# Optimization experiments

Measured on AMD Instinct MI355X. Metric: run time of the kernel, lower is better.

Reference implementation:

```python
import jax, jax.numpy as jnp
import numpy as np

N, E, G, S = 200000, 800000, 2048, 128
NUM_OPS, NUM_ETYPES, NUMERIC = 64, 4, 12
H, TEXT, VOCAB, OUT = 256, 64, 30000, 512
IN0 = 32 + NUMERIC  # 44


def _ln(h, eps=1e-5):
    # nn.LayerNorm with default (ones/zeros) affine, created fresh each forward
    m = h.mean(-1, keepdims=True)
    v = ((h - m) ** 2).mean(-1, keepdims=True)
    return (h - m) * jax.lax.rsqrt(v + eps)


def _leaky(v):
    return jnp.where(v > 0, v, 0.1 * v)  # LeakyReLU(0.1)


def setup_inputs() -> dict:
    key = jax.random.key(0)
    ks = jax.random.split(key, 40)
    x = jax.random.normal(ks[0], (N, 1 + NUMERIC), jnp.float32)
    x = x.at[:, 0].set(jax.random.randint(ks[1], (N,), 0, NUM_OPS).astype(jnp.float32))
    inp = {
        'x': x,
        'edge_index': jax.random.randint(ks[2], (2, E), 0, N),
        'edge_attr': jax.random.randint(ks[3], (E,), 0, NUM_ETYPES),
        'batch': jnp.sort(jax.random.randint(ks[4], (N,), 0, G)),
        'sql_ids': jax.random.randint(ks[5], (G, S), 0, VOCAB),
        'sql_mask': (jax.random.uniform(ks[6], (G, S)) > 0.3).astype(jnp.float32),
        'op_embed': jax.random.normal(ks[7], (NUM_OPS, 32), jnp.float32),
        'edge_embed': jax.random.normal(ks[8], (NUM_ETYPES, 16), jnp.float32),
        'token_embed': jax.random.normal(ks[9], (VOCAB, TEXT), jnp.float32).at[0].set(0.0),  # padding_idx=0
    }
    dims = [IN0, H, H]
    k = 10
    for i, d in enumerate(dims):
        inp[f'lin_w{i}'] = jax.random.normal(ks[k], (d, 16), jnp.float32) * 0.05; k += 1
        inp[f'lin_b{i}'] = jnp.zeros((d,), jnp.float32)
        inp[f'eps{i}'] = jnp.zeros((), jnp.float32)  # train_eps init 0
        inp[f'W1_{i}'] = jax.random.normal(ks[k], (H, d), jnp.float32) * 0.05; k += 1
        inp[f'b1_{i}'] = jnp.zeros((H,), jnp.float32)
        inp[f'W2_{i}'] = jax.random.normal(ks[k], (H, H), jnp.float32) * 0.05; k += 1
        inp[f'b2_{i}'] = jnp.zeros((H,), jnp.float32)
    inp['mW1'] = jax.random.normal(ks[k], (H, H + 3 + TEXT), jnp.float32) * 0.05; k += 1
    inp['mb1'] = jnp.zeros((H,), jnp.float32)
    inp['mW2'] = jax.random.normal(ks[k], (OUT, H), jnp.float32) * 0.05
    inp['mb2'] = jnp.zeros((OUT,), jnp.float32)
    return inp


def reference(x, edge_index, edge_attr, batch, sql_ids, sql_mask,
              op_embed, edge_embed, token_embed,
              lin_w0, lin_b0, eps0, W1_0, b1_0, W2_0, b2_0,
              lin_w1, lin_b1, eps1, W1_1, b1_1, W2_1, b2_1,
              lin_w2, lin_b2, eps2, W1_2, b1_2, W2_2, b2_2,
              mW1, mb1, mW2, mb2):
    op_ids = jnp.clip(x[:, 0].astype(jnp.int32), 0, NUM_OPS - 1)
    nums = x[:, 1:]
    e_idx = jnp.minimum(edge_attr, NUM_ETYPES - 1)  # clamp_max
    edge_emb = edge_embed[e_idx]                    # [E,16]
    h = jnp.concatenate([op_embed[op_ids], nums], 1)  # [N,44]
    src, dst = edge_index[0], edge_index[1]
    convs = [(lin_w0, lin_b0, eps0, W1_0, b1_0, W2_0, b2_0),
             (lin_w1, lin_b1, eps1, W1_1, b1_1, W2_1, b2_1),
             (lin_w2, lin_b2, eps2, W1_2, b1_2, W2_2, b2_2)]
    for (lw, lb, eps, W1, b1, W2, b2) in convs:
        h_in = h
        # GINEConv: msg = relu(x_j + Lin(edge_attr)); sum-aggregate at dst
        msg = jax.nn.relu(h[src] + edge_emb @ lw.T + lb)        # [E,d]
        aggr = jax.ops.segment_sum(msg, dst, num_segments=h.shape[0])
        z = (1.0 + eps) * h + aggr
        h = jax.nn.relu(z @ W1.T + b1) @ W2.T + b2              # conv MLP -> [N,H]
        h = _ln(h)
        h = _leaky(h + h_in) if h_in.shape[-1] == h.shape[-1] else _leaky(h)
    # graph pooling
    g = jax.ops.segment_sum(h, batch, num_segments=G)            # global_add_pool
    count = jax.ops.segment_sum(jnp.ones((h.shape[0],), h.dtype), batch, num_segments=G)
    denom = jnp.maximum(count, 1.0)                              # scatter_mean semantics
    fanout_mean = jax.ops.segment_sum(x[:, 5], batch, num_segments=G) / denom
    cost_mean = jax.ops.segment_sum(x[:, 4], batch, num_segments=G) / denom
    graph_sum = jnp.stack([count, fanout_mean, cost_mean], 1)    # [G,3]
    # text pooling (masked mean)
    emb = token_embed[sql_ids]                                   # [G,S,TEXT]
    summed = (emb * sql_mask[..., None]).sum(1)
    lengths = jnp.maximum(sql_mask.sum(1, keepdims=True), 1.0)
    text_feat = summed / lengths
    cat = jnp.concatenate([g, graph_sum, text_feat], 1)          # [G, H+3+TEXT]
    hid = _leaky(cat @ mW1.T + mb1)                              # Dropout(0.1) is identity in eval
    return hid @ mW2.T + mb2                                     # [G, OUT]
```

## Files before the change

kernel.cpp:

```cpp
#include <hip/hip_runtime.h>

#define NN 200000
#define EE 800000
#define GG 2048
#define NBLK ((NN + 255) / 256)

typedef __attribute__((ext_vector_type(8))) short short8;
typedef __attribute__((ext_vector_type(4))) float f32x4;

__device__ __forceinline__ float bf2f(ushort u){
  unsigned x = ((unsigned)u) << 16;
  return __uint_as_float(x);
}
__device__ __forceinline__ ushort f2bf(float f){
  unsigned x = __float_as_uint(f);
  x += 0x7fffu + ((x >> 16) & 1u);
  return (ushort)(x >> 16);
}
__device__ __forceinline__ void pkAddBf16(ushort* addr, unsigned val){
  asm volatile("global_atomic_pk_add_bf16 %0, %1, off" : : "v"(addr), "v"(val) : "memory");
}

__device__ __forceinline__ void swz256(const float* __restrict__ W, ushort* __restrict__ o, int idx){
  int ks = idx >> 13, rem = idx & 8191;
  int j16 = rem >> 9, rem2 = rem & 511;
  int ln = rem2 >> 3, t = rem2 & 7;
  int row = j16*16 + (ln & 15);
  int k = ks*32 + (ln >> 4)*8 + t;
  o[idx] = f2bf(W[(size_t)row*256 + k]);
}

__global__ __launch_bounds__(256) void prep_k(
    const float* __restrict__ W10, const float* __restrict__ W20,
    const float* __restrict__ W11, const float* __restrict__ W21,
    const float* __restrict__ W12, const float* __restrict__ W22,
    const float* __restrict__ lw0, const float* __restrict__ lb0,
    const float* __restrict__ lw1, const float* __restrict__ lb1,
    const float* __restrict__ lw2, const float* __restrict__ lb2,
    const float* __restrict__ eE, const float* __restrict__ mW1,
    const float* __restrict__ mW2,
    ushort* __restrict__ wb10, ushort* __restrict__ wb20,
    ushort* __restrict__ wb11, ushort* __restrict__ wb21,
    ushort* __restrict__ wb12, ushort* __restrict__ wb22,
    ushort* __restrict__ mW1b, ushort* __restrict__ mW2b,
    float* __restrict__ eb)
{
  int b = blockIdx.x, tid = threadIdx.x;
  if (b < 64){
    int idx = b*256 + tid;
    int ks = idx >> 13, rem = idx & 8191;
    int j16 = rem >> 9, rem2 = rem & 511;
    int ln = rem2 >> 3, t = rem2 & 7;
    int row = j16*16 + (ln & 15);
    int k = ks*32 + (ln >> 4)*8 + t;
    wb10[idx] = (k < 44) ? f2bf(W10[row*44 + k]) : (ushort)0;
    return;
  }
  b -= 64;
  if (b < 256){ swz256(W20, wb20, b*256+tid); return; } b -= 256;
  if (b < 256){ swz256(W11, wb11, b*256+tid); return; } b -= 256;
  if (b < 256){ swz256(W21, wb21, b*256+tid); return; } b -= 256;
  if (b < 256){ swz256(W12, wb12, b*256+tid); return; } b -= 256;
  if (b < 256){ swz256(W22, wb22, b*256+tid); return; } b -= 256;
  if (b < 384){
    int idx = b*256 + tid; int o = idx / 384, k = idx - o*384;
    mW1b[idx] = (k < 323) ? f2bf(mW1[(size_t)o*323 + k]) : (ushort)0;
    return;
  }
  b -= 384;
  if (b < 512){ int idx = b*256+tid; mW2b[idx] = f2bf(mW2[idx]); return; } b -= 512;
  int li = b >> 2, t = b & 3;
  const float* lw = (li == 0) ? lw0 : ((li == 1) ? lw1 : lw2);
  const float* lb = (li == 0) ? lb0 : ((li == 1) ? lb1 : lb2);
  int d = (li == 0) ? 44 : 256;
  float v = 0.f;
  if (tid < d){
    float a = 0.f;
    #pragma unroll
    for (int j = 0; j < 16; j++) a += eE[t*16 + j] * lw[tid*16 + j];
    v = a + lb[tid];
  }
  eb[(li*4 + t)*256 + tid] = v;
}

__global__ __launch_bounds__(256) void build_h0_k(
    const float* __restrict__ x, const float* __restrict__ opE, ushort* __restrict__ h0)
{
  int idx = blockIdx.x*256 + threadIdx.x;
  int i = idx >> 6, c = idx & 63;
  float v = 0.f;
  if (c < 32){
    int op = (int)x[(size_t)i*13];
    op = op < 0 ? 0 : (op > 63 ? 63 : op);
    v = opE[op*32 + c];
  } else if (c < 44){
    v = x[(size_t)i*13 + (c - 31)];
  }
  h0[idx] = f2bf(v);
}

__global__ __launch_bounds__(256) void deg_k(const int* __restrict__ dst, int* __restrict__ D){
  int e = blockIdx.x*256 + threadIdx.x;
  atomicAdd(&D[dst[e]], 1);
}
__global__ __launch_bounds__(256) void scan1_k(int* __restrict__ D, int* __restrict__ bsum){
  __shared__ int s[256];
  int b = blockIdx.x, t = threadIdx.x, idx = b*256 + t;
  int v = (idx < NN) ? D[idx] : 0;
  s[t] = v; __syncthreads();
  for (int off = 1; off < 256; off <<= 1){
    int u = (t >= off) ? s[t-off] : 0;
    __syncthreads();
    s[t] += u;
    __syncthreads();
  }
  if (idx < NN) D[idx] = s[t] - v;
  if (t == 255) bsum[b] = s[255];
}
__global__ __launch_bounds__(256) void scan2_k(int* __restrict__ bsum){
  __shared__ int s[256];
  __shared__ int carry;
  int t = threadIdx.x;
  if (t == 0) carry = 0;
  __syncthreads();
  for (int c0 = 0; c0 < NBLK; c0 += 256){
    int idx = c0 + t;
    int v = (idx < NBLK) ? bsum[idx] : 0;
    s[t] = v; __syncthreads();
    for (int off = 1; off < 256; off <<= 1){
      int u = (t >= off) ? s[t-off] : 0;
      __syncthreads();
      s[t] += u;
      __syncthreads();
    }
    int ex = s[t] - v + carry;
    if (idx < NBLK) bsum[idx] = ex;
    int tot = s[255];
    __syncthreads();
    if (t == 0) carry += tot;
    __syncthreads();
  }
}
__global__ __launch_bounds__(256) void scan3_k(int* __restrict__ D, const int* __restrict__ bsum){
  int b = blockIdx.x, idx = b*256 + threadIdx.x;
  if (idx < NN) D[idx] += bsum[b];
}
__global__ __launch_bounds__(256) void fill_k(const int* __restrict__ src, const int* __restrict__ dst,
                                              const int* __restrict__ et, int* __restrict__ D,
                                              int* __restrict__ csr){
  int e = blockIdx.x*256 + threadIdx.x;
  int d = dst[e];
  int t = et[e]; t = t < 3 ? t : 3;
  int pos = atomicAdd(&D[d], 1);
  csr[pos] = src[e] | (t << 18);
}

__global__ __launch_bounds__(256) void gather256_k(
    const ushort* __restrict__ h, const int* __restrict__ Dend, const int* __restrict__ csr,
    const float* __restrict__ eb, ushort* __restrict__ aggr)
{
  __shared__ float ebs[1024];
  int tid = threadIdx.x;
  for (int i = tid; i < 1024; i += 256) ebs[i] = eb[i];
  __syncthreads();
  int r = blockIdx.x*4 + (tid >> 6);
  int lane = tid & 63;
  int c = lane * 4;
  int start = (r == 0) ? 0 : Dend[r-1];
  int end = Dend[r];
  float a0 = 0.f, a1 = 0.f, a2 = 0.f, a3 = 0.f;
  for (int e = start; e < end; e++){
    int p = csr[e];
    int s = p & 0x3FFFF;
    int t = p >> 18;
    const ushort4 hv = *(const ushort4*)(h + (size_t)s*256 + c);
    const float4 ev = *(const float4*)&ebs[t*256 + c];
    float v;
    v = bf2f(hv.x) + ev.x; a0 += v > 0.f ? v : 0.f;
    v = bf2f(hv.y) + ev.y; a1 += v > 0.f ? v : 0.f;
    v = bf2f(hv.z) + ev.z; a2 += v > 0.f ? v : 0.f;
    v = bf2f(hv.w) + ev.w; a3 += v > 0.f ? v : 0.f;
  }
  ushort4 o; o.x = f2bf(a0); o.y = f2bf(a1); o.z = f2bf(a2); o.w = f2bf(a3);
  *(ushort4*)(aggr + (size_t)r*256 + c) = o;
}

__global__ __launch_bounds__(256) void gather44_k(
    const ushort* __restrict__ h0, const int* __restrict__ Dend, const int* __restrict__ csr,
    const float* __restrict__ eb, ushort* __restrict__ aggr)
{
  __shared__ float ebs[256];
  int tid = threadIdx.x;
  if (tid < 256) ebs[tid] = eb[(tid >> 6)*256 + (tid & 63)];
  __syncthreads();
  int wv = tid >> 6, lane = tid & 63;
  int sub = lane >> 4, lg = lane & 15;
  int r = blockIdx.x*16 + wv*4 + sub;
  int c = lg * 4;
  int start = (r == 0) ? 0 : Dend[r-1];
  int end = Dend[r];
  float a0 = 0.f, a1 = 0.f, a2 = 0.f, a3 = 0.f;
  for (int e = start; e < end; e++){
    int p = csr[e];
    int s = p & 0x3FFFF;
    int t = p >> 18;
    const ushort4 hv = *(const ushort4*)(h0 + (size_t)s*64 + c);
    const float4 ev = *(const float4*)&ebs[t*64 + c];
    float v;
    v = bf2f(hv.x) + ev.x; a0 += v > 0.f ? v : 0.f;
    v = bf2f(hv.y) + ev.y; a1 += v > 0.f ? v : 0.f;
    v = bf2f(hv.z) + ev.z; a2 += v > 0.f ? v : 0.f;
    v = bf2f(hv.w) + ev.w; a3 += v > 0.f ? v : 0.f;
  }
  ushort4 o; o.x = f2bf(a0); o.y = f2bf(a1); o.z = f2bf(a2); o.w = f2bf(a3);
  *(ushort4*)(aggr + (size_t)r*64 + c) = o;
}

__global__ __launch_bounds__(256) void msg44_k(
    const ushort* __restrict__ h0, const int* __restrict__ src, const int* __restrict__ dst,
    const int* __restrict__ et, const float* __restrict__ eb, ushort* __restrict__ aggr)
{
  int e = blockIdx.x*4 + (threadIdx.x >> 6);
  int lane = threadIdx.x & 63;
  if (lane < 22){
    int s = src[e], d = dst[e];
    int t = et[e]; t = t < 3 ? t : 3;
    int c = lane * 2;
    const ushort2 hv = *(const ushort2*)(h0 + (size_t)s*64 + c);
    float v0 = bf2f(hv.x) + eb[t*256 + c];     v0 = v0 > 0.f ? v0 : 0.f;
    float v1 = bf2f(hv.y) + eb[t*256 + c + 1]; v1 = v1 > 0.f ? v1 : 0.f;
    unsigned pv = (unsigned)f2bf(v0) | ((unsigned)f2bf(v1) << 16);
    pkAddBf16(aggr + (size_t)d*64 + c, pv);
  }
}
__global__ __launch_bounds__(256) void msg256_k(
    const ushort* __restrict__ h, const int* __restrict__ src, const int* __restrict__ dst,
    const int* __restrict__ et, const float* __restrict__ eb, ushort* __restrict__ aggr)
{
  int e = blockIdx.x*4 + (threadIdx.x >> 6);
  int lane = threadIdx.x & 63;
  int s = src[e], d = dst[e];
  int t = et[e]; t = t < 3 ? t : 3;
  int c = lane * 4;
  const ushort4 hv = *(const ushort4*)(h + (size_t)s*256 + c);
  const float4 ev = *(const float4*)(eb + t*256 + c);
  float v0 = bf2f(hv.x) + ev.x; v0 = v0 > 0.f ? v0 : 0.f;
  float v1 = bf2f(hv.y) + ev.y; v1 = v1 > 0.f ? v1 : 0.f;
  float v2 = bf2f(hv.z) + ev.z; v2 = v2 > 0.f ? v2 : 0.f;
  float v3 = bf2f(hv.w) + ev.w; v3 = v3 > 0.f ? v3 : 0.f;
  unsigned p0 = (unsigned)f2bf(v0) | ((unsigned)f2bf(v1) << 16);
  unsigned p1 = (unsigned)f2bf(v2) | ((unsigned)f2bf(v3) << 16);
  ushort* ap = aggr + (size_t)d*256 + c;
  pkAddBf16(ap, p0);
  pkAddBf16(ap + 2, p1);
}

template<int KD, int RESID>
__global__ __launch_bounds__(256) void layer_k(
    const ushort* hsrc, const ushort* __restrict__ aggr,
    const ushort* __restrict__ W1s, const float* __restrict__ b1,
    const ushort* __restrict__ W2s, const float* __restrict__ b2,
    const float* __restrict__ epsp, ushort* hout)
{
  __shared__ ushort ZT[64][264];
  __shared__ float red1[64][4], red2[64][4], mnL[64], rsL[64];
  const int tid = threadIdx.x, lane = tid & 63, wv = tid >> 6;
  const int l15 = lane & 15, lq = lane >> 4;
  const int rowBase = blockIdx.x * 64;
  const float epv = 1.0f + epsp[0];

  if (KD == 256){
    #pragma unroll
    for (int p = 0; p < 16; p++){
      int r = p*4 + (tid >> 6);
      int c = (tid & 63) * 4;
      const ushort4 hv = *(const ushort4*)(hsrc + (size_t)(rowBase + r)*256 + c);
      const ushort4 av = *(const ushort4*)(aggr + (size_t)(rowBase + r)*256 + c);
      ushort4 o;
      o.x = f2bf(epv*bf2f(hv.x) + bf2f(av.x));
      o.y = f2bf(epv*bf2f(hv.y) + bf2f(av.y));
      o.z = f2bf(epv*bf2f(hv.z) + bf2f(av.z));
      o.w = f2bf(epv*bf2f(hv.w) + bf2f(av.w));
      *(ushort4*)&ZT[r][c] = o;
    }
  } else {
    #pragma unroll
    for (int p = 0; p < 4; p++){
      int r = p*16 + (tid >> 4);
      int c = (tid & 15) * 4;
      const ushort4 hv = *(const ushort4*)(hsrc + (size_t)(rowBase + r)*64 + c);
      const ushort4 av = *(const ushort4*)(aggr + (size_t)(rowBase + r)*64 + c);
      ushort4 o;
      o.x = f2bf(epv*bf2f(hv.x) + bf2f(av.x));
      o.y = f2bf(epv*bf2f(hv.y) + bf2f(av.y));
      o.z = f2bf(epv*bf2f(hv.z) + bf2f(av.z));
      o.w = f2bf(epv*bf2f(hv.w) + bf2f(av.w));
      *(ushort4*)&ZT[r][c] = o;
    }
  }
  __syncthreads();

  f32x4 acc[4][4];
  #pragma unroll
  for (int i = 0; i < 4; i++)
    #pragma unroll
    for (int j = 0; j < 4; j++){ f32x4 z = {0.f,0.f,0.f,0.f}; acc[i][j] = z; }

  #pragma unroll
  for (int s = 0; s < KD/32; s++){
    short8 af[4], bfv[4];
    #pragma unroll
    for (int j = 0; j < 4; j++)
      bfv[j] = *(const short8*)(W1s + ((size_t)(s*16 + wv*4 + j)*64 + lane)*8);
    #pragma unroll
    for (int i = 0; i < 4; i++)
      af[i] = *(const short8*)&ZT[i*16 + l15][s*32 + lq*8];
    #pragma unroll
    for (int i = 0; i < 4; i++)
      #pragma unroll
      for (int j = 0; j < 4; j++)
        acc[i][j] = __builtin_amdgcn_mfma_f32_16x16x32_bf16(af[i], bfv[j], acc[i][j], 0, 0, 0);
  }
  __syncthreads();

  {
    float b1c[4];
    #pragma unroll
    for (int j = 0; j < 4; j++) b1c[j] = b1[wv*64 + j*16 + l15];
    #pragma unroll
    for (int i = 0; i < 4; i++)
      #pragma unroll
      for (int j = 0; j < 4; j++){
        int cc = wv*64 + j*16 + l15;
        #pragma unroll
        for (int rg = 0; rg < 4; rg++){
          int r = i*16 + (lq << 2) + rg;
          float v = acc[i][j][rg] + b1c[j];
          v = v > 0.f ? v : 0.f;
          ZT[r][cc] = f2bf(v);
        }
      }
  }
  __syncthreads();

  #pragma unroll
  for (int i = 0; i < 4; i++)
    #pragma unroll
    for (int j = 0; j < 4; j++){ f32x4 z = {0.f,0.f,0.f,0.f}; acc[i][j] = z; }

  #pragma unroll
  for (int s = 0; s < 8; s++){
    short8 af[4], bfv[4];
    #pragma unroll
    for (int j = 0; j < 4; j++)
      bfv[j] = *(const short8*)(W2s + ((size_t)(s*16 + wv*4 + j)*64 + lane)*8);
    #pragma unroll
    for (int i = 0; i < 4; i++)
      af[i] = *(const short8*)&ZT[i*16 + l15][s*32 + lq*8];
    #pragma unroll
    for (int i = 0; i < 4; i++)
      #pragma unroll
      for (int j = 0; j < 4; j++)
        acc[i][j] = __builtin_amdgcn_mfma_f32_16x16x32_bf16(af[i], bfv[j], acc[i][j], 0, 0, 0);
  }

  float b2c[4];
  #pragma unroll
  for (int j = 0; j < 4; j++) b2c[j] = b2[wv*64 + j*16 + l15];
  #pragma unroll
  for (int i = 0; i < 4; i++){
    #pragma unroll
    for (int rg = 0; rg < 4; rg++){
      float s1 = 0.f, s2 = 0.f;
      #pragma unroll
      for (int j = 0; j < 4; j++){
        float y = acc[i][j][rg] + b2c[j];
        s1 += y; s2 += y*y;
      }
      #pragma unroll
      for (int m = 1; m < 16; m <<= 1){
        s1 += __shfl_xor(s1, m, 64);
        s2 += __shfl_xor(s2, m, 64);
      }
      if (l15 == 0){
        int r = i*16 + (lq << 2) + rg;
        red1[r][wv] = s1; red2[r][wv] = s2;
      }
    }
  }
  __syncthreads();
  if (tid < 64){
    float s1 = red1[tid][0] + red1[tid][1] + red1[tid][2] + red1[tid][3];
    float s2 = red2[tid][0] + red2[tid][1] + red2[tid][2] + red2[tid][3];
    float mn = s1 * (1.f/256.f);
    float vr = s2 * (1.f/256.f) - mn*mn;
    mnL[tid] = mn;
    rsL[tid] = rsqrtf(vr + 1e-5f);
  }
  __syncthreads();
  #pragma unroll
  for (int i = 0; i < 4; i++){
    #pragma unroll
    for (int rg = 0; rg < 4; rg++){
      int r = i*16 + (lq << 2) + rg;
      float mn = mnL[r], rs = rsL[r];
      #pragma unroll
      for (int j = 0; j < 4; j++){
        int cc = wv*64 + j*16 + l15;
        float y = acc[i][j][rg] + b2c[j];
        float v = (y - mn) * rs;
        if (RESID) v += bf2f(hsrc[(size_t)(rowBase + r)*256 + cc]);
        v = v > 0.f ? v : 0.1f*v;
        ZT[r][cc] = f2bf(v);
      }
    }
  }
  __syncthreads();
  #pragma unroll
  for (int p = 0; p < 16; p++){
    int r = p*4 + (tid >> 6);
    int c = (tid & 63) * 4;
    *(ushort4*)(hout + (size_t)(rowBase + r)*256 + c) = *(const ushort4*)&ZT[r][c];
  }
}

__global__ __launch_bounds__(256) void readout_k(
    const ushort* __restrict__ h, const int* __restrict__ batch, const float* __restrict__ x,
    const int* __restrict__ sqlIds, const float* __restrict__ sqlMask,
    const float* __restrict__ tok, ushort* __restrict__ catb)
{
  int g = blockIdx.x, tid = threadIdx.x;
  __shared__ int se[2];
  __shared__ float part[4][64];
  __shared__ float mpart[4];
  if (tid < 2){
    int target = g + tid;
    int lo = 0, hi = NN;
    while (lo < hi){ int mid = (lo + hi) >> 1; if (batch[mid] < target) lo = mid + 1; else hi = mid; }
    se[tid] = lo;
  }
  __syncthreads();
  int start = se[0], end = se[1];
  float a = 0.f;
  for (int i = start; i < end; i++) a += bf2f(h[(size_t)i*256 + tid]);
  catb[(size_t)g*384 + tid] = f2bf(a);
  if (tid < 2){
    int col = (tid == 0) ? 5 : 4;
    float s = 0.f;
    for (int i = start; i < end; i++) s += x[(size_t)i*13 + col];
    float cnt = (float)(end - start);
    float dn = cnt > 1.f ? cnt : 1.f;
    if (tid == 0){ catb[(size_t)g*384 + 256] = f2bf(cnt); catb[(size_t)g*384 + 257] = f2bf(s / dn); }
    else { catb[(size_t)g*384 + 258] = f2bf(s / dn); }
  }
  int grp = tid >> 6, c = tid & 63;
  float acc = 0.f, m = 0.f;
  for (int s = grp; s < 128; s += 4){
    int id = sqlIds[g*128 + s];
    float mk = sqlMask[g*128 + s];
    m += mk;
    acc += tok[(size_t)id*64 + c] * mk;
  }
  part[grp][c] = acc;
  if (c == 0) mpart[grp] = m;
  __syncthreads();
  if (tid < 64){
    float L = mpart[0] + mpart[1] + mpart[2] + mpart[3];
    L = L > 1.f ? L : 1.f;
    float tsum = part[0][tid] + part[1][tid] + part[2][tid] + part[3][tid];
    catb[(size_t)g*384 + 259 + tid] = f2bf(tsum / L);
  }
  if (tid >= 64 && tid < 125){
    catb[(size_t)g*384 + 259 + tid] = 0;
  }
}

__global__ __launch_bounds__(256) void head1_k(
    const ushort* __restrict__ catb, const ushort* __restrict__ W1b,
    const float* __restrict__ b1, ushort* __restrict__ hidb)
{
  __shared__ ushort smem[64*72 + 256*72];
  ushort (*As)[72] = (ushort(*)[72])smem;
  ushort (*Ws)[72] = (ushort(*)[72])(smem + 64*72);
  const int tid = threadIdx.x, lane = tid & 63, wv = tid >> 6;
  const int rowBase = blockIdx.x * 64;
  f32x4 acc[4][4];
  #pragma unroll
  for (int i = 0; i < 4; i++)
    #pragma unroll
    for (int j = 0; j < 4; j++){ f32x4 z = {0.f,0.f,0.f,0.f}; acc[i][j] = z; }

  for (int k0 = 0; k0 < 384; k0 += 64){
    __syncthreads();
    #pragma unroll
    for (int p = 0; p < 4; p++){
      int r = p*16 + (tid >> 4);
      int kk = (tid & 15) * 4;
      *(ushort4*)&As[r][kk] = *(const ushort4*)(catb + (size_t)(rowBase + r)*384 + k0 + kk);
    }
    #pragma unroll
    for (int p = 0; p < 16; p++){
      int oc = p*16 + (tid >> 4);
      int kk = (tid & 15) * 4;
      *(ushort4*)&Ws[oc][kk] = *(const ushort4*)(W1b + (size_t)oc*384 + k0 + kk);
    }
    __syncthreads();
    #pragma unroll
    for (int kc = 0; kc < 2; kc++){
      short8 af[4], bfv[4];
      #pragma unroll
      for (int i = 0; i < 4; i++)
        af[i] = *(const short8*)&As[i*16 + (lane & 15)][kc*32 + (lane >> 4)*8];
      #pragma unroll
      for (int j = 0; j < 4; j++)
        bfv[j] = *(const short8*)&Ws[wv*64 + j*16 + (lane & 15)][kc*32 + (lane >> 4)*8];
      #pragma unroll
      for (int i = 0; i < 4; i++)
        #pragma unroll
        for (int j = 0; j < 4; j++)
          acc[i][j] = __builtin_amdgcn_mfma_f32_16x16x32_bf16(af[i], bfv[j], acc[i][j], 0, 0, 0);
    }
  }
  __syncthreads();
  ushort (*Cs)[264] = (ushort(*)[264])smem;
  #pragma unroll
  for (int j = 0; j < 4; j++){
    int cc = wv*64 + j*16 + (lane & 15);
    float bb = b1[cc];
    #pragma unroll
    for (int i = 0; i < 4; i++){
      #pragma unroll
      for (int rg = 0; rg < 4; rg++){
        int r = i*16 + ((lane >> 4) << 2) + rg;
        float v = acc[i][j][rg] + bb;
        v = v > 0.f ? v : 0.1f*v;
        Cs[r][cc] = f2bf(v);
      }
    }
  }
  __syncthreads();
  #pragma unroll
  for (int p = 0; p < 16; p++){
    int r = p*4 + (tid >> 6);
    int c = (tid & 63) * 4;
    *(ushort4*)(hidb + (size_t)(rowBase + r)*256 + c) = *(const ushort4*)&Cs[r][c];
  }
}

__global__ __launch_bounds__(256) void head2_k(
    const ushort* __restrict__ hidb, const ushort* __restrict__ W2b,
    const float* __restrict__ b2, float* __restrict__ out)
{
  __shared__ float smemf[128*132];
  ushort (*As)[72] = (ushort(*)[72])smemf;
  ushort (*Bs)[72] = (ushort(*)[72])((ushort*)smemf + 128*72);
  const int tid = threadIdx.x, lane = tid & 63, wv = tid >> 6;
  const int wr = (wv >> 1) * 64;
  const int wc = (wv & 1) * 64;
  const int rowBase = blockIdx.x * 128;
  const int colBase = blockIdx.y * 128;
  const int lr = tid >> 4, lk = (tid & 15) * 4;

  f32x4 acc[4][4];
  #pragma unroll
  for (int i = 0; i < 4; i++)
    #pragma unroll
    for (int j = 0; j < 4; j++){ f32x4 z = {0.f,0.f,0.f,0.f}; acc[i][j] = z; }

  for (int k0 = 0; k0 < 256; k0 += 64){
    __syncthreads();
    #pragma unroll
    for (int p = 0; p < 8; p++){
      int r = lr + p*16;
      *(ushort4*)&As[r][lk] = *(const ushort4*)(hidb + (size_t)(rowBase + r)*256 + k0 + lk);
      *(ushort4*)&Bs[r][lk] = *(const ushort4*)(W2b + (size_t)(colBase + r)*256 + k0 + lk);
    }
    __syncthreads();
    #pragma unroll
    for (int kc = 0; kc < 2; kc++){
      short8 af[4], bfv[4];
      #pragma unroll
      for (int i = 0; i < 4; i++)
        af[i] = *(const short8*)&As[wr + i*16 + (lane & 15)][kc*32 + (lane >> 4)*8];
      #pragma unroll
      for (int j = 0; j < 4; j++)
        bfv[j] = *(const short8*)&Bs[wc + j*16 + (lane & 15)][kc*32 + (lane >> 4)*8];
      #pragma unroll
      for (int i = 0; i < 4; i++)
        #pragma unroll
        for (int j = 0; j < 4; j++)
          acc[i][j] = __builtin_amdgcn_mfma_f32_16x16x32_bf16(af[i], bfv[j], acc[i][j], 0, 0, 0);
    }
  }
  __syncthreads();
  float (*Cs)[132] = (float(*)[132])smemf;
  #pragma unroll
  for (int j = 0; j < 4; j++){
    int cl = wc + j*16 + (lane & 15);
    float bb = b2[colBase + cl];
    #pragma unroll
    for (int i = 0; i < 4; i++){
      int r0 = wr + i*16 + ((lane >> 4) << 2);
      #pragma unroll
      for (int rg = 0; rg < 4; rg++)
        Cs[r0 + rg][cl] = acc[i][j][rg] + bb;
    }
  }
  __syncthreads();
  #pragma unroll
  for (int p = 0; p < 16; p++){
    int r = (tid >> 5) + p*8;
    int c4 = (tid & 31) * 4;
    *(float4*)(out + (size_t)(rowBase + r)*512 + colBase + c4) = *(const float4*)&Cs[r][c4];
  }
}

extern "C" void kernel_launch(void* const* d_in, const int* in_sizes, int n_in,
                              void* d_out, int out_size, void* d_ws, size_t ws_size,
                              hipStream_t stream)
{
  const float* x       = (const float*)d_in[0];
  const int*   ei      = (const int*)d_in[1];
  const int*   src     = ei;
  const int*   dst     = ei + EE;
  const int*   eattr   = (const int*)d_in[2];
  const int*   batch   = (const int*)d_in[3];
  const int*   sqlIds  = (const int*)d_in[4];
  const float* sqlMask = (const float*)d_in[5];
  const float* opE     = (const float*)d_in[6];
  const float* eE      = (const float*)d_in[7];
  const float* tok     = (const float*)d_in[8];
  const float* lw0 = (const float*)d_in[9],  *lb0 = (const float*)d_in[10], *eps0 = (const float*)d_in[11];
  const float* W10 = (const float*)d_in[12], *b10 = (const float*)d_in[13];
  const float* W20 = (const float*)d_in[14], *b20 = (const float*)d_in[15];
  const float* lw1 = (const float*)d_in[16], *lb1 = (const float*)d_in[17], *eps1 = (const float*)d_in[18];
  const float* W11 = (const float*)d_in[19], *b11 = (const float*)d_in[20];
  const float* W21 = (const float*)d_in[21], *b21 = (const float*)d_in[22];
  const float* lw2 = (const float*)d_in[23], *lb2 = (const float*)d_in[24], *eps2 = (const float*)d_in[25];
  const float* W12 = (const float*)d_in[26], *b12 = (const float*)d_in[27];
  const float* W22 = (const float*)d_in[28], *b22 = (const float*)d_in[29];
  const float* mW1 = (const float*)d_in[30], *mb1 = (const float*)d_in[31];
  const float* mW2 = (const float*)d_in[32], *mb2 = (const float*)d_in[33];
  float* out = (float*)d_out;

  char* ws = (char*)d_ws;
  size_t off = 0;
  const size_t NB256 = (size_t)NN*256*2;
  ushort* bufH    = (ushort*)(ws + off); off += NB256;
  char*   region  = ws + off;            off += NB256;
  ushort* h0      = (ushort*)region;
  ushort* aggr64  = (ushort*)(region + (size_t)NN*64*2);
  ushort* aggr256 = (ushort*)region;
  ushort* catb    = (ushort*)region;
  ushort* hidb    = (ushort*)(region + (size_t)GG*384*2);
  ushort* wb10 = (ushort*)(ws + off); off += (size_t)256*64*2;
  ushort* wb20 = (ushort*)(ws + off); off += (size_t)65536*2;
  ushort* wb11 = (ushort*)(ws + off); off += (size_t)65536*2;
  ushort* wb21 = (ushort*)(ws + off); off += (size_t)65536*2;
  ushort* wb12 = (ushort*)(ws + off); off += (size_t)65536*2;
  ushort* wb22 = (ushort*)(ws + off); off += (size_t)65536*2;
  ushort* mW1b = (ushort*)(ws + off); off += (size_t)256*384*2;
  ushort* mW2b = (ushort*)(ws + off); off += (size_t)512*256*2;
  float*  eb   = (float*)(ws + off);  off += (size_t)3*4*256*4;
  size_t needBase = off;
  int* D    = (int*)(ws + off); off += (size_t)NN*4;
  int* bsum = (int*)(ws + off); off += (size_t)NBLK*4;
  int* csr  = (int*)(ws + off); off += (size_t)EE*4;
  size_t needFast = off;

  if (ws_size < needBase) return;
  const bool fast = (ws_size >= needFast);

  prep_k<<<2252, 256, 0, stream>>>(W10, W20, W11, W21, W12, W22,
                                   lw0, lb0, lw1, lb1, lw2, lb2, eE, mW1, mW2,
                                   wb10, wb20, wb11, wb21, wb12, wb22, mW1b, mW2b, eb);
  build_h0_k<<<50000, 256, 0, stream>>>(x, opE, h0);

  if (fast){
    hipMemsetAsync(D, 0, (size_t)NN*4, stream);
    deg_k<<<3125, 256, 0, stream>>>(dst, D);
    scan1_k<<<NBLK, 256, 0, stream>>>(D, bsum);
    scan2_k<<<1, 256, 0, stream>>>(bsum);
    scan3_k<<<NBLK, 256, 0, stream>>>(D, bsum);
    fill_k<<<3125, 256, 0, stream>>>(src, dst, eattr, D, csr);

    gather44_k<<<12500, 256, 0, stream>>>(h0, D, csr, eb, aggr64);
    layer_k<64,0><<<3125, 256, 0, stream>>>(h0, aggr64, wb10, b10, wb20, b20, eps0, bufH);
    gather256_k<<<50000, 256, 0, stream>>>(bufH, D, csr, eb + 1024, aggr256);
    layer_k<256,1><<<3125, 256, 0, stream>>>(bufH, aggr256, wb11, b11, wb21, b21, eps1, bufH);
    gather256_k<<<50000, 256, 0, stream>>>(bufH, D, csr, eb + 2048, aggr256);
    layer_k<256,1><<<3125, 256, 0, stream>>>(bufH, aggr256, wb12, b12, wb22, b22, eps2, bufH);
  } else {
    hipMemsetAsync(aggr64, 0, (size_t)NN*64*2, stream);
    msg44_k<<<EE/4, 256, 0, stream>>>(h0, src, dst, eattr, eb, aggr64);
    layer_k<64,0><<<3125, 256, 0, stream>>>(h0, aggr64, wb10, b10, wb20, b20, eps0, bufH);

    hipMemsetAsync(aggr256, 0, NB256, stream);
    msg256_k<<<EE/4, 256, 0, stream>>>(bufH, src, dst, eattr, eb + 1024, aggr256);
    layer_k<256,1><<<3125, 256, 0, stream>>>(bufH, aggr256, wb11, b11, wb21, b21, eps1, bufH);

    hipMemsetAsync(aggr256, 0, NB256, stream);
    msg256_k<<<EE/4, 256, 0, stream>>>(bufH, src, dst, eattr, eb + 2048, aggr256);
    layer_k<256,1><<<3125, 256, 0, stream>>>(bufH, aggr256, wb12, b12, wb22, b22, eps2, bufH);
  }

  readout_k<<<GG, 256, 0, stream>>>(bufH, batch, x, sqlIds, sqlMask, tok, catb);
  head1_k<<<32, 256, 0, stream>>>(catb, mW1b, mb1, hidb);
  head2_k<<<dim3(16, 4), 256, 0, stream>>>(hidb, mW2b, mb2, out);
}
```

Before: 1.019 ms.

## Fuse CSR neighbor gather into GIN layer MLP kernel with ping-pong buffers

New measurement: 960.7 us. -5.7%, faster.

```diff
diff --git a/kernel.cpp b/kernel.cpp
--- a/kernel.cpp
+++ b/kernel.cpp
@@ -16,9 +16,6 @@
   unsigned x = __float_as_uint(f);
   x += 0x7fffu + ((x >> 16) & 1u);
   return (ushort)(x >> 16);
-}
-__device__ __forceinline__ void pkAddBf16(ushort* addr, unsigned val){
-  asm volatile("global_atomic_pk_add_bf16 %0, %1, off" : : "v"(addr), "v"(val) : "memory");
 }
 
 __device__ __forceinline__ void swz256(const float* __restrict__ W, ushort* __restrict__ o, int idx){
@@ -155,168 +152,105 @@
   csr[pos] = src[e] | (t << 18);
 }
 
-__global__ __launch_bounds__(256) void gather256_k(
-    const ushort* __restrict__ h, const int* __restrict__ Dend, const int* __restrict__ csr,
-    const float* __restrict__ eb, ushort* __restrict__ aggr)
-{
-  __shared__ float ebs[1024];
-  int tid = threadIdx.x;
-  for (int i = tid; i < 1024; i += 256) ebs[i] = eb[i];
-  __syncthreads();
-  int r = blockIdx.x*4 + (tid >> 6);
-  int lane = tid & 63;
-  int c = lane * 4;
-  int start = (r == 0) ? 0 : Dend[r-1];
-  int end = Dend[r];
-  float a0 = 0.f, a1 = 0.f, a2 = 0.f, a3 = 0.f;
-  for (int e = start; e < end; e++){
-    int p = csr[e];
-    int s = p & 0x3FFFF;
-    int t = p >> 18;
-    const ushort4 hv = *(const ushort4*)(h + (size_t)s*256 + c);
-    const float4 ev = *(const float4*)&ebs[t*256 + c];
-    float v;
-    v = bf2f(hv.x) + ev.x; a0 += v > 0.f ? v : 0.f;
-    v = bf2f(hv.y) + ev.y; a1 += v > 0.f ? v : 0.f;
-    v = bf2f(hv.z) + ev.z; a2 += v > 0.f ? v : 0.f;
-    v = bf2f(hv.w) + ev.w; a3 += v > 0.f ? v : 0.f;
-  }
-  ushort4 o; o.x = f2bf(a0); o.y = f2bf(a1); o.z = f2bf(a2); o.w = f2bf(a3);
-  *(ushort4*)(aggr + (size_t)r*256 + c) = o;
-}
-
-__global__ __launch_bounds__(256) void gather44_k(
-    const ushort* __restrict__ h0, const int* __restrict__ Dend, const int* __restrict__ csr,
-    const float* __restrict__ eb, ushort* __restrict__ aggr)
-{
-  __shared__ float ebs[256];
-  int tid = threadIdx.x;
-  if (tid < 256) ebs[tid] = eb[(tid >> 6)*256 + (tid & 63)];
-  __syncthreads();
-  int wv = tid >> 6, lane = tid & 63;
-  int sub = lane >> 4, lg = lane & 15;
-  int r = blockIdx.x*16 + wv*4 + sub;
-  int c = lg * 4;
-  int start = (r == 0) ? 0 : Dend[r-1];
-  int end = Dend[r];
-  float a0 = 0.f, a1 = 0.f, a2 = 0.f, a3 = 0.f;
-  for (int e = start; e < end; e++){
-    int p = csr[e];
-    int s = p & 0x3FFFF;
-    int t = p >> 18;
-    const ushort4 hv = *(const ushort4*)(h0 + (size_t)s*64 + c);
-    const float4 ev = *(const float4*)&ebs[t*64 + c];
-    float v;
-    v = bf2f(hv.x) + ev.x; a0 += v > 0.f ? v : 0.f;
-    v = bf2f(hv.y) + ev.y; a1 += v > 0.f ? v : 0.f;
-    v = bf2f(hv.z) + ev.z; a2 += v > 0.f ? v : 0.f;
-    v = bf2f(hv.w) + ev.w; a3 += v > 0.f ? v : 0.f;
-  }
-  ushort4 o; o.x = f2bf(a0); o.y = f2bf(a1); o.z = f2bf(a2); o.w = f2bf(a3);
-  *(ushort4*)(aggr + (size_t)r*64 + c) = o;
-}
-
-__global__ __launch_bounds__(256) void msg44_k(
-    const ushort* __restrict__ h0, const int* __restrict__ src, const int* __restrict__ dst,
-    const int* __restrict__ et, const float* __restrict__ eb, ushort* __restrict__ aggr)
-{
-  int e = blockIdx.x*4 + (threadIdx.x >> 6);
-  int lane = threadIdx.x & 63;
-  if (lane < 22){
-    int s = src[e], d = dst[e];
-    int t = et[e]; t = t < 3 ? t : 3;
-    int c = lane * 2;
-    const ushort2 hv = *(const ushort2*)(h0 + (size_t)s*64 + c);
-    float v0 = bf2f(hv.x) + eb[t*256 + c];     v0 = v0 > 0.f ? v0 : 0.f;
-    float v1 = bf2f(hv.y) + eb[t*256 + c + 1]; v1 = v1 > 0.f ? v1 : 0.f;
-    unsigned pv = (unsigned)f2bf(v0) | ((unsigned)f2bf(v1) << 16);
-    pkAddBf16(aggr + (size_t)d*64 + c, pv);
-  }
-}
-__global__ __launch_bounds__(256) void msg256_k(
-    const ushort* __restrict__ h, const int* __restrict__ src, const int* __restrict__ dst,
-    const int* __restrict__ et, const float* __restrict__ eb, ushort* __restrict__ aggr)
-{
-  int e = blockIdx.x*4 + (threadIdx.x >> 6);
-  int lane = threadIdx.x & 63;
-  int s = src[e], d = dst[e];
-  int t = et[e]; t = t < 3 ? t : 3;
-  int c = lane * 4;
-  const ushort4 hv = *(const ushort4*)(h + (size_t)s*256 + c);
-  const float4 ev = *(const float4*)(eb + t*256 + c);
-  float v0 = bf2f(hv.x) + ev.x; v0 = v0 > 0.f ? v0 : 0.f;
-  float v1 = bf2f(hv.y) + ev.y; v1 = v1 > 0.f ? v1 : 0.f;
-  float v2 = bf2f(hv.z) + ev.z; v2 = v2 > 0.f ? v2 : 0.f;
-  float v3 = bf2f(hv.w) + ev.w; v3 = v3 > 0.f ? v3 : 0.f;
-  unsigned p0 = (unsigned)f2bf(v0) | ((unsigned)f2bf(v1) << 16);
-  unsigned p1 = (unsigned)f2bf(v2) | ((unsigned)f2bf(v3) << 16);
-  ushort* ap = aggr + (size_t)d*256 + c;
-  pkAddBf16(ap, p0);
-  pkAddBf16(ap + 2, p1);
-}
-
 template<int KD, int RESID>
-__global__ __launch_bounds__(256) void layer_k(
-    const ushort* hsrc, const ushort* __restrict__ aggr,
+__global__ __launch_bounds__(256) void layerf_k(
+    const ushort* __restrict__ hsrc, const int* __restrict__ Dend, const int* __restrict__ csr,
+    const float* __restrict__ ebL,
     const ushort* __restrict__ W1s, const float* __restrict__ b1,
     const ushort* __restrict__ W2s, const float* __restrict__ b2,
-    const float* __restrict__ epsp, ushort* hout)
+    const float* __restrict__ epsp, ushort* __restrict__ hout)
 {
-  __shared__ ushort ZT[64][264];
-  __shared__ float red1[64][4], red2[64][4], mnL[64], rsL[64];
+  __shared__ ushort ZT[32][264];
+  __shared__ float ebs[1024];
+  __shared__ float red1[32][4], red2[32][4], mnL[32], rsL[32];
   const int tid = threadIdx.x, lane = tid & 63, wv = tid >> 6;
   const int l15 = lane & 15, lq = lane >> 4;
-  const int rowBase = blockIdx.x * 64;
+  const int rowBase = blockIdx.x * 32;
   const float epv = 1.0f + epsp[0];
 
+  for (int i = tid; i < 1024; i += 256) ebs[i] = ebL[i];
+  __syncthreads();
+
   if (KD == 256){
-    #pragma unroll
-    for (int p = 0; p < 16; p++){
-      int r = p*4 + (tid >> 6);
-      int c = (tid & 63) * 4;
-      const ushort4 hv = *(const ushort4*)(hsrc + (size_t)(rowBase + r)*256 + c);
-      const ushort4 av = *(const ushort4*)(aggr + (size_t)(rowBase + r)*256 + c);
-      ushort4 o;
-      o.x = f2bf(epv*bf2f(hv.x) + bf2f(av.x));
-      o.y = f2bf(epv*bf2f(hv.y) + bf2f(av.y));
-      o.z = f2bf(epv*bf2f(hv.z) + bf2f(av.z));
-      o.w = f2bf(epv*bf2f(hv.w) + bf2f(av.w));
-      *(ushort4*)&ZT[r][c] = o;
+    int c = lane * 4;
+    #pragma unroll 1
+    for (int it = 0; it < 8; it++){
+      int rr = wv*8 + it;
+      int r = rowBase + rr;
+      const ushort4 hv = *(const ushort4*)(hsrc + (size_t)r*256 + c);
+      float a0 = epv*bf2f(hv.x), a1 = epv*bf2f(hv.y), a2 = epv*bf2f(hv.z), a3 = epv*bf2f(hv.w);
+      int st = (r == 0) ? 0 : Dend[r-1];
+      int en = Dend[r];
+      if (st < en){
+        int p = csr[st];
+        ushort4 sv = *(const ushort4*)(hsrc + (size_t)(p & 0x3FFFF)*256 + c);
+        int tt = (p >> 18)*256;
+        for (int e = st; e < en; e++){
+          ushort4 cur = sv; int tc = tt;
+          int e2 = (e+1 < en) ? e+1 : e;
+          int p2 = csr[e2];
+          sv = *(const ushort4*)(hsrc + (size_t)(p2 & 0x3FFFF)*256 + c);
+          tt = (p2 >> 18)*256;
+          float v;
+          v = bf2f(cur.x) + ebs[tc + c];     a0 += v > 0.f ? v : 0.f;
+          v = bf2f(cur.y) + ebs[tc + c + 1]; a1 += v > 0.f ? v : 0.f;
+          v = bf2f(cur.z) + ebs[tc + c + 2]; a2 += v > 0.f ? v : 0.f;
+          v = bf2f(cur.w) + ebs[tc + c + 3]; a3 += v > 0.f ? v : 0.f;
+        }
+      }
+      ushort4 o; o.x=f2bf(a0); o.y=f2bf(a1); o.z=f2bf(a2); o.w=f2bf(a3);
+      *(ushort4*)&ZT[rr][c] = o;
     }
   } else {
-    #pragma unroll
-    for (int p = 0; p < 4; p++){
-      int r = p*16 + (tid >> 4);
-      int c = (tid & 15) * 4;
-      const ushort4 hv = *(const ushort4*)(hsrc + (size_t)(rowBase + r)*64 + c);
-      const ushort4 av = *(const ushort4*)(aggr + (size_t)(rowBase + r)*64 + c);
-      ushort4 o;
-      o.x = f2bf(epv*bf2f(hv.x) + bf2f(av.x));
-      o.y = f2bf(epv*bf2f(hv.y) + bf2f(av.y));
-      o.z = f2bf(epv*bf2f(hv.z) + bf2f(av.z));
-      o.w = f2bf(epv*bf2f(hv.w) + bf2f(av.w));
-      *(ushort4*)&ZT[r][c] = o;
-    }
-  }
-  __syncthreads();
-
-  f32x4 acc[4][4];
-  #pragma unroll
-  for (int i = 0; i < 4; i++)
+    int c = l15 * 4;
+    #pragma unroll 1
+    for (int it = 0; it < 2; it++){
+      int rr = wv*8 + it*4 + lq;
+      int r = rowBase + rr;
+      const ushort4 hv = *(const ushort4*)(hsrc + (size_t)r*64 + c);
+      float a0 = epv*bf2f(hv.x), a1 = epv*bf2f(hv.y), a2 = epv*bf2f(hv.z), a3 = epv*bf2f(hv.w);
+      int st = (r == 0) ? 0 : Dend[r-1];
+      int en = Dend[r];
+      if (st < en){
+        int p = csr[st];
+        ushort4 sv = *(const ushort4*)(hsrc + (size_t)(p & 0x3FFFF)*64 + c);
+        int tt = (p >> 18)*256;
+        for (int e = st; e < en; e++){
+          ushort4 cur = sv; int tc = tt;
+          int e2 = (e+1 < en) ? e+1 : e;
+          int p2 = csr[e2];
+          sv = *(const ushort4*)(hsrc + (size_t)(p2 & 0x3FFFF)*64 + c);
+          tt = (p2 >> 18)*256;
+          float v;
+          v = bf2f(cur.x) + ebs[tc + c];     a0 += v > 0.f ? v : 0.f;
+          v = bf2f(cur.y) + ebs[tc + c + 1]; a1 += v > 0.f ? v : 0.f;
+          v = bf2f(cur.z) + ebs[tc + c + 2]; a2 += v > 0.f ? v : 0.f;
+          v = bf2f(cur.w) + ebs[tc + c + 3]; a3 += v > 0.f ? v : 0.f;
+        }
+      }
+      ushort4 o; o.x=f2bf(a0); o.y=f2bf(a1); o.z=f2bf(a2); o.w=f2bf(a3);
+      *(ushort4*)&ZT[rr][c] = o;
+    }
+  }
+  __syncthreads();
+
+  f32x4 acc[2][4];
+  #pragma unroll
+  for (int i = 0; i < 2; i++)
     #pragma unroll
     for (int j = 0; j < 4; j++){ f32x4 z = {0.f,0.f,0.f,0.f}; acc[i][j] = z; }
 
   #pragma unroll
   for (int s = 0; s < KD/32; s++){
-    short8 af[4], bfv[4];
+    short8 af[2], bfv[4];
     #pragma unroll
     for (int j = 0; j < 4; j++)
       bfv[j] = *(const short8*)(W1s + ((size_t)(s*16 + wv*4 + j)*64 + lane)*8);
     #pragma unroll
-    for (int i = 0; i < 4; i++)
+    for (int i = 0; i < 2; i++)
       af[i] = *(const short8*)&ZT[i*16 + l15][s*32 + lq*8];
     #pragma unroll
-    for (int i = 0; i < 4; i++)
+    for (int i = 0; i < 2; i++)
       #pragma unroll
       for (int j = 0; j < 4; j++)
         acc[i][j] = __builtin_amdgcn_mfma_f32_16x16x32_bf16(af[i], bfv[j], acc[i][j], 0, 0, 0);
@@ -328,7 +262,7 @@
     #pragma unroll
     for (int j = 0; j < 4; j++) b1c[j] = b1[wv*64 + j*16 + l15];
     #pragma unroll
-    for (int i = 0; i < 4; i++)
+    for (int i = 0; i < 2; i++)
       #pragma unroll
       for (int j = 0; j < 4; j++){
         int cc = wv*64 + j*16 + l15;
@@ -344,21 +278,21 @@
   __syncthreads();
 
   #pragma unroll
-  for (int i = 0; i < 4; i++)
+  for (int i = 0; i < 2; i++)
     #pragma unroll
     for (int j = 0; j < 4; j++){ f32x4 z = {0.f,0.f,0.f,0.f}; acc[i][j] = z; }
 
   #pragma unroll
   for (int s = 0; s < 8; s++){
-    short8 af[4], bfv[4];
+    short8 af[2], bfv[4];
     #pragma unroll
     for (int j = 0; j < 4; j++)
       bfv[j] = *(const short8*)(W2s + ((size_t)(s*16 + wv*4 + j)*64 + lane)*8);
     #pragma unroll
-    for (int i = 0; i < 4; i++)
+    for (int i = 0; i < 2; i++)
       af[i] = *(const short8*)&ZT[i*16 + l15][s*32 + lq*8];
     #pragma unroll
-    for (int i = 0; i < 4; i++)
+    for (int i = 0; i < 2; i++)
       #pragma unroll
       for (int j = 0; j < 4; j++)
         acc[i][j] = __builtin_amdgcn_mfma_f32_16x16x32_bf16(af[i], bfv[j], acc[i][j], 0, 0, 0);
@@ -368,7 +302,7 @@
   #pragma unroll
   for (int j = 0; j < 4; j++) b2c[j] = b2[wv*64 + j*16 + l15];
   #pragma unroll
-  for (int i = 0; i < 4; i++){
+  for (int i = 0; i < 2; i++){
     #pragma unroll
     for (int rg = 0; rg < 4; rg++){
       float s1 = 0.f, s2 = 0.f;
@@ -389,7 +323,7 @@
     }
   }
   __syncthreads();
-  if (tid < 64){
+  if (tid < 32){
     float s1 = red1[tid][0] + red1[tid][1] + red1[tid][2] + red1[tid][3];
     float s2 = red2[tid][0] + red2[tid][1] + red2[tid][2] + red2[tid][3];
     float mn = s1 * (1.f/256.f);
@@ -399,7 +333,7 @@
   }
   __syncthreads();
   #pragma unroll
-  for (int i = 0; i < 4; i++){
+  for (int i = 0; i < 2; i++){
     #pragma unroll
     for (int rg = 0; rg < 4; rg++){
       int r = i*16 + (lq << 2) + rg;
@@ -417,7 +351,7 @@
   }
   __syncthreads();
   #pragma unroll
-  for (int p = 0; p < 16; p++){
+  for (int p = 0; p < 8; p++){
     int r = p*4 + (tid >> 6);
     int c = (tid & 63) * 4;
     *(ushort4*)(hout + (size_t)(rowBase + r)*256 + c) = *(const ushort4*)&ZT[r][c];
@@ -649,8 +583,7 @@
   ushort* bufH    = (ushort*)(ws + off); off += NB256;
   char*   region  = ws + off;            off += NB256;
   ushort* h0      = (ushort*)region;
-  ushort* aggr64  = (ushort*)(region + (size_t)NN*64*2);
-  ushort* aggr256 = (ushort*)region;
+  ushort* hPong   = (ushort*)region;
   ushort* catb    = (ushort*)region;
   ushort* hidb    = (ushort*)(region + (size_t)GG*384*2);
   ushort* wb10 = (ushort*)(ws + off); off += (size_t)256*64*2;
@@ -662,47 +595,28 @@
   ushort* mW1b = (ushort*)(ws + off); off += (size_t)256*384*2;
   ushort* mW2b = (ushort*)(ws + off); off += (size_t)512*256*2;
   float*  eb   = (float*)(ws + off);  off += (size_t)3*4*256*4;
-  size_t needBase = off;
   int* D    = (int*)(ws + off); off += (size_t)NN*4;
   int* bsum = (int*)(ws + off); off += (size_t)NBLK*4;
   int* csr  = (int*)(ws + off); off += (size_t)EE*4;
   size_t needFast = off;
 
-  if (ws_size < needBase) return;
-  const bool fast = (ws_size >= needFast);
+  if (ws_size < needFast) return;
 
   prep_k<<<2252, 256, 0, stream>>>(W10, W20, W11, W21, W12, W22,
                                    lw0, lb0, lw1, lb1, lw2, lb2, eE, mW1, mW2,
                                    wb10, wb20, wb11, wb21, wb12, wb22, mW1b, mW2b, eb);
   build_h0_k<<<50000, 256, 0, stream>>>(x, opE, h0);
 
-  if (fast){
-    hipMemsetAsync(D, 0, (size_t)NN*4, stream);
-    deg_k<<<3125, 256, 0, stream>>>(dst, D);
-    scan1_k<<<NBLK, 256, 0, stream>>>(D, bsum);
-    scan2_k<<<1, 256, 0, stream>>>(bsum);
-    scan3_k<<<NBLK, 256, 0, stream>>>(D, bsum);
-    fill_k<<<3125, 256, 0, stream>>>(src, dst, eattr, D, csr);
-
-    gather44_k<<<12500, 256, 0, stream>>>(h0, D, csr, eb, aggr64);
-    layer_k<64,0><<<3125, 256, 0, stream>>>(h0, aggr64, wb10, b10, wb20, b20, eps0, bufH);
-    gather256_k<<<50000, 256, 0, stream>>>(bufH, D, csr, eb + 1024, aggr256);
-    layer_k<256,1><<<3125, 256, 0, stream>>>(bufH, aggr256, wb11, b11, wb21, b21, eps1, bufH);
-    gather256_k<<<50000, 256, 0, stream>>>(bufH, D, csr, eb + 2048, aggr256);
-    layer_k<256,1><<<3125, 256, 0, stream>>>(bufH, aggr256, wb12, b12, wb22, b22, eps2, bufH);
-  } else {
-    hipMemsetAsync(aggr64, 0, (size_t)NN*64*2, stream);
-    msg44_k<<<EE/4, 256, 0, stream>>>(h0, src, dst, eattr, eb, aggr64);
-    layer_k<64,0><<<3125, 256, 0, stream>>>(h0, aggr64, wb10, b10, wb20, b20, eps0, bufH);
-
-    hipMemsetAsync(aggr256, 0, NB256, stream);
-    msg256_k<<<EE/4, 256, 0, stream>>>(bufH, src, dst, eattr, eb + 1024, aggr256);
-    layer_k<256,1><<<3125, 256, 0, stream>>>(bufH, aggr256, wb11, b11, wb21, b21, eps1, bufH);
-
-    hipMemsetAsync(aggr256, 0, NB256, stream);
-    msg256_k<<<EE/4, 256, 0, stream>>>(bufH, src, dst, eattr, eb + 2048, aggr256);
-    layer_k<256,1><<<3125, 256, 0, stream>>>(bufH, aggr256, wb12, b12, wb22, b22, eps2, bufH);
-  }
+  hipMemsetAsync(D, 0, (size_t)NN*4, stream);
+  deg_k<<<3125, 256, 0, stream>>>(dst, D);
+  scan1_k<<<NBLK, 256, 0, stream>>>(D, bsum);
+  scan2_k<<<1, 256, 0, stream>>>(bsum);
+  scan3_k<<<NBLK, 256, 0, stream>>>(D, bsum);
+  fill_k<<<3125, 256, 0, stream>>>(src, dst, eattr, D, csr);
+
+  layerf_k<64,0><<<6250, 256, 0, stream>>>(h0,    D, csr, eb,        wb10, b10, wb20, b20, eps0, bufH);
+  layerf_k<256,1><<<6250, 256, 0, stream>>>(bufH, D, csr, eb + 1024, wb11, b11, wb21, b21, eps1, hPong);
+  layerf_k<256,1><<<6250, 256, 0, stream>>>(hPong,D, csr, eb + 2048, wb12, b12, wb22, b22, eps2, bufH);
 
   readout_k<<<GG, 256, 0, stream>>>(bufH, batch, x, sqlIds, sqlMask, tok, catb);
   head1_k<<<32, 256, 0, stream>>>(catb, mW1b, mb1, hidb);
```
